# Performance work log

Hardware: AMD Instinct MI355X
Metric: run time of the kernel (lower is better)

Reference implementation:

```python
import jax, jax.numpy as jnp
import numpy as np

B, S, D, O, E = 8, 4096, 1024, 1024, 64

def setup_inputs() -> dict:
    key = jax.random.key(0)
    kx, kgw, kgb, kew, keb = jax.random.split(key, 5)
    x = jax.random.normal(kx, (B, S, D), dtype=jnp.float32)
    gate_w = jax.random.normal(kgw, (E, D), dtype=jnp.float32) * 0.02
    gate_b = jnp.zeros((E,), dtype=jnp.float32)
    expert_w = jax.random.normal(kew, (E, D, O), dtype=jnp.float32) * 0.02
    expert_b = jnp.zeros((E, O), dtype=jnp.float32)
    return {"x": x, "gate_w": gate_w, "gate_b": gate_b,
            "expert_w": expert_w, "expert_b": expert_b}

def reference(x, gate_w, gate_b, expert_w, expert_b):
    # x: [B,S,D] -> flatten tokens. With world_size=1 the all-reduce and
    # all-to-alls in the torch module are identities, and per-chunk processing
    # is token-independent, so one global pass is mathematically identical.
    b, s, d = x.shape
    xt = x.reshape(-1, d)                                   # [N, D]
    logits = xt @ gate_w.T + gate_b                         # [N, E]
    gates = jax.nn.softmax(logits, axis=-1)
    sel = jnp.argmax(gates, axis=-1)                        # [N] top-1 expert
    order = jnp.argsort(sel)                                # stable sort by expert
    xs = xt[order]                                          # tokens grouped by expert
    counts = jnp.bincount(sel, length=E).astype(jnp.int32)  # tokens per expert
    # Grouped expert GEMM: row block e of xs multiplies expert_w[e].
    ys = jax.lax.ragged_dot(xs, expert_w, counts)           # [N, O]
    ys = ys + expert_b[sel[order]]
    # Combine: scatter sorted outputs back to original token positions.
    # (Note: torch output is NOT scaled by gate probability.)
    out = jnp.zeros((xt.shape[0], expert_w.shape[-1]), dtype=ys.dtype)
    out = out.at[order].set(ys)
    return out.reshape(b, s, -1)
```

## Files before the change

### kernel.cpp

```cpp
#include <hip/hip_runtime.h>
#include <hip/hip_bf16.h>

#define N_TOK 32768
#define DIM 1024
#define OUTD 1024
#define NEXP 64

typedef __attribute__((ext_vector_type(4))) float f32x4;
typedef __attribute__((ext_vector_type(8))) short bf16x8;

__device__ __forceinline__ unsigned short f2bf(float f) {
    unsigned int u = __builtin_bit_cast(unsigned int, f);
    u += 0x7FFFu + ((u >> 16) & 1u);
    return (unsigned short)(u >> 16);
}

#define GLOAD16(gp, lp) \
    __builtin_amdgcn_global_load_lds((const __attribute__((address_space(1))) void*)(gp), \
                                     (__attribute__((address_space(3))) void*)(lp), 16, 0, 0)

__global__ __launch_bounds__(256) void prep_kernel(const float* __restrict__ x,
        const float* __restrict__ gw, const float* __restrict__ gb,
        const float* __restrict__ ew,
        int* __restrict__ sel, int* __restrict__ nflag, int* __restrict__ flags,
        int* __restrict__ counts,
        unsigned short* __restrict__ xb, unsigned short* __restrict__ wt)
{
    __shared__ __align__(16) char smem[18688];
    int tid = threadIdx.x;

    if (blockIdx.x < 512) {
        float (*xs)[36]  = (float(*)[36])smem;
        float (*wsm)[36] = (float(*)[36])(smem + 9216);
        int* h = (int*)(smem + 18432);
        if (tid < NEXP) h[tid] = 0;
        int t0 = blockIdx.x * 64;
        int tg = tid >> 4, eg = tid & 15;

        float acc[4][4];
#pragma unroll
        for (int i = 0; i < 4; i++)
#pragma unroll
            for (int j = 0; j < 4; j++) acc[i][j] = 0.f;

        for (int k0 = 0; k0 < DIM; k0 += 32) {
            __syncthreads();
#pragma unroll
            for (int q = 0; q < 2; q++) {
                int cidx = tid + q * 256;
                int r = cidx >> 3, c4 = (cidx & 7) * 4;
                *reinterpret_cast<float4*>(&xs[r][c4]) =
                    *reinterpret_cast<const float4*>(&x[(size_t)(t0 + r) * DIM + k0 + c4]);
                *reinterpret_cast<float4*>(&wsm[r][c4]) =
                    *reinterpret_cast<const float4*>(&gw[(size_t)r * DIM + k0 + c4]);
            }
            __syncthreads();
            if (xb) {
                int r = tid >> 2, cc = (tid & 3) * 8;
                float4 v0 = *reinterpret_cast<const float4*>(&xs[r][cc]);
                float4 v1 = *reinterpret_cast<const float4*>(&xs[r][cc + 4]);
                uint4 p;
                p.x = (unsigned int)f2bf(v0.x) | ((unsigned int)f2bf(v0.y) << 16);
                p.y = (unsigned int)f2bf(v0.z) | ((unsigned int)f2bf(v0.w) << 16);
                p.z = (unsigned int)f2bf(v1.x) | ((unsigned int)f2bf(v1.y) << 16);
                p.w = (unsigned int)f2bf(v1.z) | ((unsigned int)f2bf(v1.w) << 16);
                *reinterpret_cast<uint4*>(&xb[(size_t)(t0 + r) * DIM + k0 + cc]) = p;
            }
#pragma unroll
            for (int kk4 = 0; kk4 < 8; kk4++) {
                float4 xv[4], wv[4];
#pragma unroll
                for (int i = 0; i < 4; i++)
                    xv[i] = *reinterpret_cast<const float4*>(&xs[tg + 16 * i][kk4 * 4]);
#pragma unroll
                for (int j = 0; j < 4; j++)
                    wv[j] = *reinterpret_cast<const float4*>(&wsm[eg + 16 * j][kk4 * 4]);
#pragma unroll
                for (int i = 0; i < 4; i++)
#pragma unroll
                    for (int j = 0; j < 4; j++) {
                        acc[i][j] = fmaf(xv[i].x, wv[j].x, acc[i][j]);
                        acc[i][j] = fmaf(xv[i].y, wv[j].y, acc[i][j]);
                        acc[i][j] = fmaf(xv[i].z, wv[j].z, acc[i][j]);
                        acc[i][j] = fmaf(xv[i].w, wv[j].w, acc[i][j]);
                    }
            }
        }
#pragma unroll
        for (int j = 0; j < 4; j++) {
            float b = gb[eg + 16 * j];
#pragma unroll
            for (int i = 0; i < 4; i++) acc[i][j] += b;
        }
#pragma unroll
        for (int i = 0; i < 4; i++) {
            float m1 = -1e30f, m2 = -1e30f; int e1 = 0;
#pragma unroll
            for (int j = 0; j < 4; j++) {
                float v = acc[i][j]; int e = eg + 16 * j;
                if (v > m1) { m2 = m1; m1 = v; e1 = e; }
                else if (v > m2) m2 = v;
            }
#pragma unroll
            for (int d = 1; d < 16; d <<= 1) {
                float om1 = __shfl_xor(m1, d, 16);
                float om2 = __shfl_xor(m2, d, 16);
                int   oe1 = __shfl_xor(e1, d, 16);
                if (om1 > m1 || (om1 == m1 && oe1 < e1)) {
                    m2 = fmaxf(om2, m1); m1 = om1; e1 = oe1;
                } else {
                    m2 = fmaxf(m2, om1);
                }
            }
            if (eg == 0) {
                int t = t0 + tg + 16 * i;
                sel[t] = e1;
                atomicAdd(&h[e1], 1);
                if (m1 - m2 < 1e-3f) {
                    int idx = atomicAdd(nflag, 1);
                    if (idx < 4096) flags[idx] = t;
                }
            }
        }
        __syncthreads();
        if (tid < NEXP && h[tid]) atomicAdd(&counts[tid], h[tid]);
    } else {
        if (!wt) return;
        unsigned short* ts = (unsigned short*)smem;
        int lin = blockIdx.x - 512;
        int e = lin >> 8;
        int d0 = (lin & 15) * 64, o0 = ((lin >> 4) & 15) * 64;
        const float* src = ew + (size_t)e * (DIM * OUTD);
        int og = tid & 7;
        int dl = tid >> 3;
#pragma unroll
        for (int i = 0; i < 2; i++) {
            int d = dl + 32 * i;
            const float* sr = &src[(size_t)(d0 + d) * OUTD + o0 + og * 8];
            float4 v0 = *reinterpret_cast<const float4*>(sr);
            float4 v1 = *reinterpret_cast<const float4*>(sr + 4);
            unsigned short b[8] = { f2bf(v0.x), f2bf(v0.y), f2bf(v0.z), f2bf(v0.w),
                                    f2bf(v1.x), f2bf(v1.y), f2bf(v1.z), f2bf(v1.w) };
            int dg = d >> 3, dr = d & 7;
#pragma unroll
            for (int k = 0; k < 8; k++) {
                int o = og * 8 + k;
                int key = (o & 7) ^ ((o >> 3) & 7);
                ts[o * 72 + ((dg ^ key) << 3) + dr] = b[k];
            }
        }
        __syncthreads();
        unsigned short* dst = wt + (size_t)e * (DIM * OUTD);
        int dc = tid & 7;
        int ol = tid >> 3;
#pragma unroll
        for (int i = 0; i < 2; i++) {
            int o = ol + 32 * i;
            int key = (o & 7) ^ ((o >> 3) & 7);
            uint4 v = *reinterpret_cast<const uint4*>(&ts[o * 72 + ((dc ^ key) << 3)]);
            *reinterpret_cast<uint4*>(&dst[(size_t)(o0 + o) * DIM + d0 + dc * 8]) = v;
        }
    }
}

__global__ __launch_bounds__(64) void gate_fix_kernel(const float* __restrict__ x,
        const float* __restrict__ gw, const float* __restrict__ gb,
        int* __restrict__ sel, const int* __restrict__ nflag, const int* __restrict__ flags,
        int* __restrict__ counts)
{
    int n = *nflag; if (n > 4096) n = 4096;
    int b = blockIdx.x;
    if (b >= n) return;
    int t = flags[b];
    int e = threadIdx.x;
    const float* xr = x + (size_t)t * DIM;
    const float* wr = gw + (size_t)e * DIM;
    double acc = (double)gb[e];
    for (int k = 0; k < DIM; k += 4) {
        acc += (double)xr[k]   * (double)wr[k];
        acc += (double)xr[k+1] * (double)wr[k+1];
        acc += (double)xr[k+2] * (double)wr[k+2];
        acc += (double)xr[k+3] * (double)wr[k+3];
    }
    double m1 = acc; int e1 = e;
#pragma unroll
    for (int d = 1; d < 64; d <<= 1) {
        double om1 = __shfl_xor(m1, d, 64);
        int   oe1  = __shfl_xor(e1, d, 64);
        if (om1 > m1 || (om1 == m1 && oe1 < e1)) { m1 = om1; e1 = oe1; }
    }
    if (e == 0) {
        int eOld = sel[t];
        if (eOld != e1) {
            sel[t] = e1;
            atomicSub(&counts[eOld], 1);
            atomicAdd(&counts[e1], 1);
        }
    }
}

__global__ void sched_kernel(const int* __restrict__ counts, int* __restrict__ offsets,
                             int* __restrict__ schedE, int* __restrict__ schedR,
                             int* __restrict__ totalRB, int rowsShift)
{
    int e = threadIdx.x;
    int c = counts[e];
    int v = c;
#pragma unroll
    for (int d = 1; d < 64; d <<= 1) { int y = __shfl_up(v, d, 64); if (e >= d) v += y; }
    offsets[e] = v - c;
    if (e == 63) offsets[NEXP] = v;
    int rows = 1 << rowsShift;
    int nb = (c + rows - 1) >> rowsShift;
    int rbv = nb;
#pragma unroll
    for (int d = 1; d < 64; d <<= 1) { int y = __shfl_up(rbv, d, 64); if (e >= d) rbv += y; }
    int rbBase = rbv - nb;
    for (int i = 0; i < nb; i++) { schedE[rbBase + i] = e; schedR[rbBase + i] = i << rowsShift; }
    if (e == 63) *totalRB = rbv;
}

__global__ __launch_bounds__(256) void scatter_kernel(const int* __restrict__ sel,
        const int* __restrict__ offsets, int* __restrict__ cursor, int* __restrict__ perm)
{
    int t = blockIdx.x * 256 + threadIdx.x;
    int e = sel[t];
    int pos = offsets[e] + atomicAdd(&cursor[e], 1);
    perm[pos] = t;
}

__global__ __launch_bounds__(512, 4) void moe_gemm6(
        const unsigned short* __restrict__ xb, const unsigned short* __restrict__ wt,
        const float* __restrict__ eb,
        const int* __restrict__ perm, const int* __restrict__ offsets,
        const int* __restrict__ counts, const int* __restrict__ schedE,
        const int* __restrict__ schedR, const int* __restrict__ totalRB,
        float* __restrict__ out)
{
    int idx = blockIdx.x;
    int xcd = idx & 7;
    int s = idx >> 3;
    int cb = s & 7;
    int rb = (s >> 3) * 8 + xcd;
    if (rb >= *totalRB) return;
    int e = schedE[rb], r0 = schedR[rb];
    int cnt = counts[e], base = offsets[e];

    __shared__ __align__(16) unsigned short As[16384];
    __shared__ __align__(16) unsigned short Bs[8192];

    int tid = threadIdx.x;
    int lane = tid & 63;
    int wv = tid >> 6;
    int wr = wv >> 1, wc = wv & 1;
    int lr = lane & 15, lg = lane >> 4;

    int rowS = tid >> 2;
    int koff = ((tid & 3) ^ ((tid >> 3) & 3)) * 8;
    int rA1 = r0 + rowS, rA2 = r0 + 128 + rowS;
    int tokA1 = (rA1 < cnt) ? perm[base + rA1] : 0;
    int tokA2 = (rA2 < cnt) ? perm[base + rA2] : 0;

    const unsigned short* wte = wt + ((size_t)e << 20);
    const unsigned short* aSrc1 = xb + (size_t)tokA1 * DIM + koff;
    const unsigned short* aSrc2 = xb + (size_t)tokA2 * DIM + koff;
    const unsigned short* bSrc1 = wte + (size_t)(cb * 128 + rowS) * DIM + koff;

    unsigned short* AsQ0 = As + wv * 512;
    unsigned short* AsQ1 = As + 4096 + wv * 512;
    unsigned short* BsQ0 = Bs + wv * 512;

    f32x4 acc[4][4];
#pragma unroll
    for (int m = 0; m < 4; m++)
#pragma unroll
        for (int n = 0; n < 4; n++)
#pragma unroll
            for (int c = 0; c < 4; c++) acc[m][n][c] = 0.f;

    const char* Asc = (const char*)As;
    const char* Bsc = (const char*)Bs;
    int fko = (lg ^ ((lr >> 1) & 3)) * 16;

    auto stage = [&](int buf, int k0) {
        GLOAD16(aSrc1 + k0, AsQ0 + buf * 8192);
        GLOAD16(aSrc2 + k0, AsQ1 + buf * 8192);
        GLOAD16(bSrc1 + k0, BsQ0 + buf * 4096);
    };
    auto compute = [&](int buf) {
        int aoff = buf * 16384;
        int boff = buf * 8192;
        bf16x8 bfr[4];
#pragma unroll
        for (int n = 0; n < 4; n++) {
            int row = wc * 64 + n * 16 + lr;
            bfr[n] = *reinterpret_cast<const bf16x8*>(Bsc + boff + (row << 6) + fko);
        }
        __builtin_amdgcn_s_setprio(1);
#pragma unroll
        for (int m = 0; m < 4; m++) {
            int row = wr * 64 + m * 16 + lr;
            bf16x8 afr = *reinterpret_cast<const bf16x8*>(Asc + aoff + (row << 6) + fko);
#pragma unroll
            for (int n = 0; n < 4; n++)
                acc[m][n] = __builtin_amdgcn_mfma_f32_16x16x32_bf16(afr, bfr[n], acc[m][n], 0, 0, 0);
        }
        __builtin_amdgcn_s_setprio(0);
    };

    stage(0, 0);
    stage(1, 32);

#pragma unroll 1
    for (int t = 0; t < 30; ++t) {
        asm volatile("s_waitcnt vmcnt(3)" ::: "memory");
        __builtin_amdgcn_s_barrier();
        compute(t & 1);
        __builtin_amdgcn_s_barrier();
        stage(t & 1, (t + 2) * 32);
    }
    asm volatile("s_waitcnt vmcnt(3)" ::: "memory");
    __builtin_amdgcn_s_barrier();
    compute(0);
    asm volatile("s_waitcnt vmcnt(0)" ::: "memory");
    __builtin_amdgcn_s_barrier();
    compute(1);

    float bias[4];
#pragma unroll
    for (int n = 0; n < 4; n++)
        bias[n] = eb[e * OUTD + cb * 128 + wc * 64 + n * 16 + lr];
#pragma unroll
    for (int m = 0; m < 4; m++) {
        int rowLoc = wr * 64 + m * 16 + lg * 4;
#pragma unroll
        for (int i2 = 0; i2 < 4; i2++) {
            int r = r0 + rowLoc + i2;
            if (r < cnt) {
                int tk = perm[base + r];
#pragma unroll
                for (int n = 0; n < 4; n++) {
                    int oc = cb * 128 + wc * 64 + n * 16 + lr;
                    out[(size_t)tk * OUTD + oc] = acc[m][n][i2] + bias[n];
                }
            }
        }
    }
}

__global__ __launch_bounds__(256) void moe_gemm_legacy(const float* __restrict__ x,
        const float* __restrict__ ew, const float* __restrict__ eb,
        const int* __restrict__ perm, const int* __restrict__ offsets,
        const int* __restrict__ counts, const int* __restrict__ schedE,
        const int* __restrict__ schedR, const int* __restrict__ totalRB,
        float* __restrict__ out)
{
    int rb = blockIdx.x;
    if (rb >= *totalRB) return;
    int cb = blockIdx.y;
    int e = schedE[rb], r0 = schedR[rb];
    int cnt = counts[e], base = offsets[e];

    __shared__ __align__(16) unsigned short As[128][40];
    __shared__ __align__(16) unsigned short Bs[128][40];
    __shared__ int toks[128];

    int tid = threadIdx.x;
    if (tid < 128) {
        int r = r0 + tid;
        toks[tid] = (r < cnt) ? perm[base + r] : -1;
    }
    __syncthreads();

    int lane = tid & 63;
    int wave = tid >> 6;
    int wr = wave >> 1, wc = wave & 1;
    int lr = lane & 15, lg = lane >> 4;

    f32x4 acc[4][4];
#pragma unroll
    for (int m = 0; m < 4; m++)
#pragma unroll
        for (int n = 0; n < 4; n++)
#pragma unroll
            for (int c = 0; c < 4; c++) acc[m][n][c] = 0.f;

    int aRow[4]; int aTok[4];
#pragma unroll
    for (int q = 0; q < 4; q++) {
        aRow[q] = (tid >> 3) + q * 32;
        int tk = toks[aRow[q]];
        aTok[q] = (tk < 0) ? 0 : tk;
    }
    int ac4 = tid & 7;
    int d0 = (tid >> 5) * 4;
    int o_lane = tid & 31;
    const float* wb = ew + (size_t)e * (DIM * OUTD) + (size_t)cb * 128;

    for (int k0 = 0; k0 < DIM; k0 += 32) {
        float4 av[4];
#pragma unroll
        for (int q = 0; q < 4; q++)
            av[q] = *reinterpret_cast<const float4*>(&x[(size_t)aTok[q] * DIM + k0 + ac4 * 4]);
        float bv[4][4];
#pragma unroll
        for (int i2 = 0; i2 < 4; i2++)
#pragma unroll
            for (int j = 0; j < 4; j++)
                bv[i2][j] = wb[(size_t)(k0 + d0 + i2) * OUTD + o_lane + 32 * j];

        __syncthreads();
#pragma unroll
        for (int q = 0; q < 4; q++) {
            uint2 p;
            p.x = (unsigned int)f2bf(av[q].x) | ((unsigned int)f2bf(av[q].y) << 16);
            p.y = (unsigned int)f2bf(av[q].z) | ((unsigned int)f2bf(av[q].w) << 16);
            *reinterpret_cast<uint2*>(&As[aRow[q]][ac4 * 4]) = p;
        }
#pragma unroll
        for (int j = 0; j < 4; j++) {
            uint2 p;
            p.x = (unsigned int)f2bf(bv[0][j]) | ((unsigned int)f2bf(bv[1][j]) << 16);
            p.y = (unsigned int)f2bf(bv[2][j]) | ((unsigned int)f2bf(bv[3][j]) << 16);
            *reinterpret_cast<uint2*>(&Bs[o_lane + 32 * j][d0]) = p;
        }
        __syncthreads();

        bf16x8 bfr[4];
#pragma unroll
        for (int n = 0; n < 4; n++)
            bfr[n] = *reinterpret_cast<const bf16x8*>(&Bs[wc * 64 + n * 16 + lr][lg * 8]);
#pragma unroll
        for (int m = 0; m < 4; m++) {
            bf16x8 afr = *reinterpret_cast<const bf16x8*>(&As[wr * 64 + m * 16 + lr][lg * 8]);
#pragma unroll
            for (int n = 0; n < 4; n++)
                acc[m][n] = __builtin_amdgcn_mfma_f32_16x16x32_bf16(afr, bfr[n], acc[m][n], 0, 0, 0);
        }
    }

#pragma unroll
    for (int n = 0; n < 4; n++) {
        int oc = cb * 128 + wc * 64 + n * 16 + lr;
        float bias = eb[e * OUTD + oc];
#pragma unroll
        for (int m = 0; m < 4; m++) {
#pragma unroll
            for (int i2 = 0; i2 < 4; i2++) {
                int rr = wr * 64 + m * 16 + lg * 4 + i2;
                int tk = toks[rr];
                if (tk >= 0)
                    out[(size_t)tk * OUTD + oc] = acc[m][n][i2] + bias;
            }
        }
    }
}

extern "C" void kernel_launch(void* const* d_in, const int* in_sizes, int n_in,
                              void* d_out, int out_size, void* d_ws, size_t ws_size,
                              hipStream_t stream)
{
    const float* x  = (const float*)d_in[0];
    const float* gw = (const float*)d_in[1];
    const float* gb = (const float*)d_in[2];
    const float* ew = (const float*)d_in[3];
    const float* eb = (const float*)d_in[4];
    float* out = (float*)d_out;

    char* ws = (char*)d_ws;
    int* counts  = (int*)(ws + 0);
    int* cursor  = (int*)(ws + 256);
    int* offsets = (int*)(ws + 512);
    int* totalRB = (int*)(ws + 1024);
    int* nflag   = (int*)(ws + 1028);
    int* flags   = (int*)(ws + 1032);
    int* schedE  = (int*)(ws + 20480);
    int* schedR  = (int*)(ws + 22528);
    int* sel     = (int*)(ws + 24576);
    int* perm    = (int*)(ws + 155648);

    const size_t WT_OFF   = (size_t)1 << 20;
    const size_t WT_BYTES = (size_t)NEXP * DIM * OUTD * 2;
    const size_t XB_OFF   = WT_OFF + WT_BYTES;
    const size_t XB_BYTES = (size_t)N_TOK * DIM * 2;
    int mode = (ws_size >= XB_OFF + XB_BYTES) ? 2 : 0;
    unsigned short* wt = (mode == 2) ? (unsigned short*)(ws + WT_OFF) : nullptr;
    unsigned short* xb = (mode == 2) ? (unsigned short*)(ws + XB_OFF) : nullptr;

    hipMemsetAsync(ws, 0, 2048, stream);

    prep_kernel<<<dim3(512 + ((mode == 2) ? 16384 : 0)), 256, 0, stream>>>(
        x, gw, gb, ew, sel, nflag, flags, counts, xb, wt);
    gate_fix_kernel<<<dim3(4096), 64, 0, stream>>>(x, gw, gb, sel, nflag, flags, counts);
    sched_kernel<<<dim3(1), 64, 0, stream>>>(counts, offsets, schedE, schedR, totalRB,
                                             (mode == 2) ? 8 : 7);
    scatter_kernel<<<dim3(N_TOK / 256), 256, 0, stream>>>(sel, offsets, cursor, perm);

    if (mode == 2)
        moe_gemm6<<<dim3(1536), 512, 0, stream>>>(xb, wt, eb, perm, offsets, counts,
                                                  schedE, schedR, totalRB, out);
    else
        moe_gemm_legacy<<<dim3(320, 8), 256, 0, stream>>>(x, ew, eb, perm, offsets, counts,
                                                          schedE, schedR, totalRB, out);
}
```

Measured before the change: 381.7 us.

## Triple-buffer GEMM LDS stages and pipeline weight transpose across fewer blocks

The grouped GEMM moves from a double-buffered to a triple-buffered LDS ring. The next stage is issued before computing the current one, which drops one barrier per K-iteration. The weight bf16 transpose in the prep kernel now runs each block over eight 64x64 tiles, prefetching the next tile into registers and alternating two LDS buffers, so launched blocks fall from 16384 to 2048. The larger LDS footprint in the GEMM may lower the number of resident blocks per CU. The fewer, longer prep blocks trade parallelism for latency hiding.

```diff
diff --git a/kernel.cpp b/kernel.cpp
--- a/kernel.cpp
+++ b/kernel.cpp
@@ -126,39 +126,66 @@
         if (tid < NEXP && h[tid]) atomicAdd(&counts[tid], h[tid]);
     } else {
         if (!wt) return;
-        unsigned short* ts = (unsigned short*)smem;
+        unsigned short* ts0 = (unsigned short*)smem;
+        unsigned short* ts1 = (unsigned short*)(smem + 9216);
         int lin = blockIdx.x - 512;
-        int e = lin >> 8;
-        int d0 = (lin & 15) * 64, o0 = ((lin >> 4) & 15) * 64;
+        int e = lin >> 5;
+        int d0 = ((lin >> 4) & 1) * 512;
+        int o0 = (lin & 15) * 64;
         const float* src = ew + (size_t)e * (DIM * OUTD);
+        unsigned short* dst = wt + (size_t)e * (DIM * OUTD);
         int og = tid & 7;
         int dl = tid >> 3;
-#pragma unroll
-        for (int i = 0; i < 2; i++) {
-            int d = dl + 32 * i;
-            const float* sr = &src[(size_t)(d0 + d) * OUTD + o0 + og * 8];
-            float4 v0 = *reinterpret_cast<const float4*>(sr);
-            float4 v1 = *reinterpret_cast<const float4*>(sr + 4);
-            unsigned short b[8] = { f2bf(v0.x), f2bf(v0.y), f2bf(v0.z), f2bf(v0.w),
-                                    f2bf(v1.x), f2bf(v1.y), f2bf(v1.z), f2bf(v1.w) };
-            int dg = d >> 3, dr = d & 7;
-#pragma unroll
-            for (int k = 0; k < 8; k++) {
-                int o = og * 8 + k;
-                int key = (o & 7) ^ ((o >> 3) & 7);
-                ts[o * 72 + ((dg ^ key) << 3) + dr] = b[k];
-            }
-        }
-        __syncthreads();
-        unsigned short* dst = wt + (size_t)e * (DIM * OUTD);
         int dc = tid & 7;
         int ol = tid >> 3;
-#pragma unroll
-        for (int i = 0; i < 2; i++) {
-            int o = ol + 32 * i;
-            int key = (o & 7) ^ ((o >> 3) & 7);
-            uint4 v = *reinterpret_cast<const uint4*>(&ts[o * 72 + ((dc ^ key) << 3)]);
-            *reinterpret_cast<uint4*>(&dst[(size_t)(o0 + o) * DIM + d0 + dc * 8]) = v;
+
+        float4 c0, c1, c2, c3;
+        {
+            const float* sr0 = &src[(size_t)(d0 + dl) * OUTD + o0 + og * 8];
+            const float* sr1 = &src[(size_t)(d0 + dl + 32) * OUTD + o0 + og * 8];
+            c0 = *reinterpret_cast<const float4*>(sr0);
+            c1 = *reinterpret_cast<const float4*>(sr0 + 4);
+            c2 = *reinterpret_cast<const float4*>(sr1);
+            c3 = *reinterpret_cast<const float4*>(sr1 + 4);
+        }
+#pragma unroll
+        for (int s = 0; s < 8; ++s) {
+            float4 n0 = c0, n1 = c1, n2 = c2, n3 = c3;
+            if (s < 7) {
+                int dsn = d0 + (s + 1) * 64;
+                const float* sr0 = &src[(size_t)(dsn + dl) * OUTD + o0 + og * 8];
+                const float* sr1 = &src[(size_t)(dsn + dl + 32) * OUTD + o0 + og * 8];
+                n0 = *reinterpret_cast<const float4*>(sr0);
+                n1 = *reinterpret_cast<const float4*>(sr0 + 4);
+                n2 = *reinterpret_cast<const float4*>(sr1);
+                n3 = *reinterpret_cast<const float4*>(sr1 + 4);
+            }
+            unsigned short* tsb = (s & 1) ? ts1 : ts0;
+#pragma unroll
+            for (int half = 0; half < 2; ++half) {
+                int dLoc = dl + 32 * half;
+                float4 va = half ? c2 : c0;
+                float4 vb = half ? c3 : c1;
+                unsigned short b[8] = { f2bf(va.x), f2bf(va.y), f2bf(va.z), f2bf(va.w),
+                                        f2bf(vb.x), f2bf(vb.y), f2bf(vb.z), f2bf(vb.w) };
+                int dg = dLoc >> 3, dr = dLoc & 7;
+#pragma unroll
+                for (int k = 0; k < 8; k++) {
+                    int o = og * 8 + k;
+                    int key = (o & 7) ^ ((o >> 3) & 7);
+                    tsb[o * 72 + ((dg ^ key) << 3) + dr] = b[k];
+                }
+            }
+            __syncthreads();
+            int ds0 = d0 + s * 64;
+#pragma unroll
+            for (int i = 0; i < 2; i++) {
+                int o = ol + 32 * i;
+                int key = (o & 7) ^ ((o >> 3) & 7);
+                uint4 v = *reinterpret_cast<const uint4*>(&tsb[o * 72 + ((dc ^ key) << 3)]);
+                *reinterpret_cast<uint4*>(&dst[(size_t)(o0 + o) * DIM + ds0 + dc * 8]) = v;
+            }
+            c0 = n0; c1 = n1; c2 = n2; c3 = n3;
         }
     }
 }
@@ -229,7 +256,7 @@
     perm[pos] = t;
 }
 
-__global__ __launch_bounds__(512, 4) void moe_gemm6(
+__global__ __launch_bounds__(512, 4) void moe_gemm7(
         const unsigned short* __restrict__ xb, const unsigned short* __restrict__ wt,
         const float* __restrict__ eb,
         const int* __restrict__ perm, const int* __restrict__ offsets,
@@ -246,8 +273,8 @@
     int e = schedE[rb], r0 = schedR[rb];
     int cnt = counts[e], base = offsets[e];
 
-    __shared__ __align__(16) unsigned short As[16384];
-    __shared__ __align__(16) unsigned short Bs[8192];
+    __shared__ __align__(16) unsigned short As[24576];
+    __shared__ __align__(16) unsigned short Bs[12288];
 
     int tid = threadIdx.x;
     int lane = tid & 63;
@@ -311,20 +338,23 @@
     stage(0, 0);
     stage(1, 32);
 
+    int cbuf = 0, sbuf = 2;
 #pragma unroll 1
     for (int t = 0; t < 30; ++t) {
         asm volatile("s_waitcnt vmcnt(3)" ::: "memory");
         __builtin_amdgcn_s_barrier();
-        compute(t & 1);
-        __builtin_amdgcn_s_barrier();
-        stage(t & 1, (t + 2) * 32);
+        stage(sbuf, (t + 2) * 32);
+        compute(cbuf);
+        cbuf = (cbuf == 2) ? 0 : cbuf + 1;
+        sbuf = (sbuf == 2) ? 0 : sbuf + 1;
     }
     asm volatile("s_waitcnt vmcnt(3)" ::: "memory");
     __builtin_amdgcn_s_barrier();
-    compute(0);
+    compute(cbuf);
+    cbuf = (cbuf == 2) ? 0 : cbuf + 1;
     asm volatile("s_waitcnt vmcnt(0)" ::: "memory");
     __builtin_amdgcn_s_barrier();
-    compute(1);
+    compute(cbuf);
 
     float bias[4];
 #pragma unroll
@@ -489,7 +519,7 @@
 
     hipMemsetAsync(ws, 0, 2048, stream);
 
-    prep_kernel<<<dim3(512 + ((mode == 2) ? 16384 : 0)), 256, 0, stream>>>(
+    prep_kernel<<<dim3(512 + ((mode == 2) ? 2048 : 0)), 256, 0, stream>>>(
         x, gw, gb, ew, sel, nflag, flags, counts, xb, wt);
     gate_fix_kernel<<<dim3(4096), 64, 0, stream>>>(x, gw, gb, sel, nflag, flags, counts);
     sched_kernel<<<dim3(1), 64, 0, stream>>>(counts, offsets, schedE, schedR, totalRB,
@@ -497,7 +527,7 @@
     scatter_kernel<<<dim3(N_TOK / 256), 256, 0, stream>>>(sel, offsets, cursor, perm);
 
     if (mode == 2)
-        moe_gemm6<<<dim3(1536), 512, 0, stream>>>(xb, wt, eb, perm, offsets, counts,
+        moe_gemm7<<<dim3(1536), 512, 0, stream>>>(xb, wt, eb, perm, offsets, counts,
                                                   schedE, schedR, totalRB, out);
     else
         moe_gemm_legacy<<<dim3(320, 8), 256, 0, stream>>>(x, ew, eb, perm, offsets, counts,
```

Measured after the change: 382.7 us. About the same (+0.3%).
